# Kernel optimization log

Hardware: AMD Instinct MI355X
Metric: run time of the kernel (lower is better)

Reference implementation:

```python
import jax, jax.numpy as jnp
import numpy as np

FP8_MAX = 448.0  # e4m3 max, from scale = max(w) / (448.0 * 6.0) in the source


def setup_inputs() -> dict:
    key = jax.random.key(0)
    k_w, k_perm, k_x, k_b = jax.random.split(key, 4)
    T, K, O = 8192, 4096, 4096  # tokens = bsz*q_len, in_features, out_features

    # --- simulate init-time reorder_quantize_w ---
    w = jax.random.normal(k_w, (O, K), dtype=jnp.float32) * 0.02
    g_scale = jnp.max(jnp.abs(w)) / (FP8_MAX * 6.0)          # global weight scale
    perm = jax.random.permutation(k_perm, K)                  # outlier reorder index
    w_r = w[:, perm] / g_scale                                # reordered, globally scaled
    scale_w = jnp.max(jnp.abs(w_r), axis=1) / FP8_MAX         # per-out-channel scale (O,)
    W = jnp.round(w_r / scale_w[:, None])                     # quantized values (stored fp32)

    # --- simulate activation quantization (same reorder applied upstream) ---
    x = jax.random.normal(k_x, (T, K), dtype=jnp.float32)
    scale_x = (jnp.max(jnp.abs(x), axis=1, keepdims=True) / FP8_MAX)  # (T,1)
    qx = jnp.round(x / scale_x)                               # quantized values (stored fp32)

    bias = jax.random.normal(k_b, (O,), dtype=jnp.float32) * 0.01
    scale = jnp.asarray([g_scale], dtype=jnp.float32)         # fused global scale (x-global * w-global)

    return {"qx": qx, "W": W, "scale_x": scale_x, "scale_w": scale_w,
            "scale": scale, "bias": bias, "bsz": 4, "q_len": 2048}


def reference(qx, W, scale_x, scale_w, scale, bias, bsz, q_len):
    # agemm.matmul: low-bit GEMM with fused per-token (scale_x), per-channel (scale_w)
    # and global (scale) dequant scales.  y[t,o] = (sum_k qx[t,k]*W[o,k]) * sx[t] * sw[o] * s
    y = jnp.einsum('tk,ok->to', qx, W)           # (T, O) accumulate
    y = y * scale_x * scale_w[None, :] * scale[0]
    y = y + bias
    return y.reshape(bsz, q_len, -1)
```

## Files before the change

kernel.cpp:

```cpp
#include <hip/hip_runtime.h>

typedef __bf16 bf16_t;
typedef __bf16 bf16x8 __attribute__((ext_vector_type(8)));
typedef __bf16 bf16x4 __attribute__((ext_vector_type(4)));
typedef float f32x4 __attribute__((ext_vector_type(4)));

constexpr int TDIM = 8192;
constexpr int KDIM = 4096;
constexpr int ODIM = 4096;
constexpr int BM = 128, BN = 128, BK = 32;

__device__ __forceinline__ void async_ld16(void* lds, const void* g) {
    __builtin_amdgcn_global_load_lds(
        (const __attribute__((address_space(1))) unsigned int*)g,
        (__attribute__((address_space(3))) unsigned int*)lds,
        16, 0, 0);
}

__global__ __launch_bounds__(256) void cvt2_kernel(const float* __restrict__ a, bf16_t* __restrict__ da,
                                                   int nblk_a,
                                                   const float* __restrict__ w, bf16_t* __restrict__ dw) {
    int b = blockIdx.x;
    const float* src;
    bf16_t* dst;
    if (b < nblk_a) { src = a; dst = da; }
    else            { src = w; dst = dw; b -= nblk_a; }
    const size_t base = (size_t)b * 2048 + threadIdx.x * 4;
    const float4 v0 = *(const float4*)(src + base);
    const float4 v1 = *(const float4*)(src + base + 1024);
    bf16x4 o0, o1;
    o0[0] = (bf16_t)v0.x; o0[1] = (bf16_t)v0.y; o0[2] = (bf16_t)v0.z; o0[3] = (bf16_t)v0.w;
    o1[0] = (bf16_t)v1.x; o1[1] = (bf16_t)v1.y; o1[2] = (bf16_t)v1.z; o1[3] = (bf16_t)v1.w;
    *(bf16x4*)(dst + base) = o0;
    *(bf16x4*)(dst + base + 1024) = o1;
}

template <bool USE_DMA>
__global__ __launch_bounds__(256, 4) void gemm_kernel(
    const bf16_t* __restrict__ A, const bf16_t* __restrict__ B,
    const float* __restrict__ Afp, const float* __restrict__ Bfp,
    const float* __restrict__ scale_x, const float* __restrict__ scale_w,
    const float* __restrict__ gscale, const float* __restrict__ bias,
    float* __restrict__ out) {
    __shared__ bf16_t sA[BM * BK];
    __shared__ bf16_t sB[BN * BK];

    const int tid = threadIdx.x;
    const int bn = blockIdx.x & 31;
    const int bm = blockIdx.x >> 5;
    const int row0 = bm * BM;
    const int col0 = bn * BN;

    const int lane = tid & 63;
    const int wid = tid >> 6;
    const int wm = (wid >> 1) * 64;
    const int wn = (wid & 1) * 64;
    const int fr = lane & 15;
    const int q  = lane >> 4;
    const int s_fr = (fr >> 1) & 3;
    const int kc = ((q ^ s_fr) * 8);

    f32x4 acc[4][4] = {};

    const int r_half = tid >> 2;
    const int c_g = (tid & 3) ^ ((tid >> 3) & 3);
    const size_t a_g = (size_t)(row0 + r_half) * KDIM + c_g * 8;
    const size_t b_g = (size_t)(col0 + r_half) * KDIM + c_g * 8;
    const int lds_off = tid * 8;

    for (int k0 = 0; k0 < KDIM; k0 += BK) {
        if (USE_DMA) {
            async_ld16(&sA[lds_off],        A + a_g + k0);
            async_ld16(&sA[2048 + lds_off], A + a_g + (size_t)64 * KDIM + k0);
            async_ld16(&sB[lds_off],        B + b_g + k0);
            async_ld16(&sB[2048 + lds_off], B + b_g + (size_t)64 * KDIM + k0);
        } else {
            const int r = tid >> 2;
            const int cg2 = (tid & 3) ^ ((tid >> 3) & 3);
#pragma unroll
            for (int h = 0; h < 2; ++h) {
                const int rr = r + h * 64;
                const float4 va0 = *(const float4*)(Afp + (size_t)(row0 + rr) * KDIM + k0 + cg2 * 8);
                const float4 va1 = *(const float4*)(Afp + (size_t)(row0 + rr) * KDIM + k0 + cg2 * 8 + 4);
                const float4 vb0 = *(const float4*)(Bfp + (size_t)(col0 + rr) * KDIM + k0 + cg2 * 8);
                const float4 vb1 = *(const float4*)(Bfp + (size_t)(col0 + rr) * KDIM + k0 + cg2 * 8 + 4);
                bf16x8 pa, pb;
                pa[0] = (bf16_t)va0.x; pa[1] = (bf16_t)va0.y; pa[2] = (bf16_t)va0.z; pa[3] = (bf16_t)va0.w;
                pa[4] = (bf16_t)va1.x; pa[5] = (bf16_t)va1.y; pa[6] = (bf16_t)va1.z; pa[7] = (bf16_t)va1.w;
                pb[0] = (bf16_t)vb0.x; pb[1] = (bf16_t)vb0.y; pb[2] = (bf16_t)vb0.z; pb[3] = (bf16_t)vb0.w;
                pb[4] = (bf16_t)vb1.x; pb[5] = (bf16_t)vb1.y; pb[6] = (bf16_t)vb1.z; pb[7] = (bf16_t)vb1.w;
                *(bf16x8*)&sA[rr * BK + (tid & 3) * 8] = pa;
                *(bf16x8*)&sB[rr * BK + (tid & 3) * 8] = pb;
            }
        }
        __syncthreads();

        bf16x8 af[4], bfr[4];
#pragma unroll
        for (int mt = 0; mt < 4; ++mt)
            af[mt] = *(const bf16x8*)&sA[(wm + mt * 16 + fr) * BK + kc];
#pragma unroll
        for (int nt = 0; nt < 4; ++nt)
            bfr[nt] = *(const bf16x8*)&sB[(wn + nt * 16 + fr) * BK + kc];
#pragma unroll
        for (int mt = 0; mt < 4; ++mt)
#pragma unroll
            for (int nt = 0; nt < 4; ++nt)
                acc[mt][nt] = __builtin_amdgcn_mfma_f32_16x16x32_bf16(af[mt], bfr[nt], acc[mt][nt], 0, 0, 0);
        __syncthreads();
    }

    const float gs = gscale[0];
    const int rbase = q * 4;
#pragma unroll
    for (int nt = 0; nt < 4; ++nt) {
        const int o = col0 + wn + nt * 16 + fr;
        const float swv = scale_w[o] * gs;
        const float bv = bias[o];
#pragma unroll
        for (int mt = 0; mt < 4; ++mt) {
#pragma unroll
            for (int i = 0; i < 4; ++i) {
                const int t = row0 + wm + mt * 16 + rbase + i;
                out[(size_t)t * ODIM + o] = acc[mt][nt][i] * (scale_x[t] * swv) + bv;
            }
        }
    }
}

extern "C" void kernel_launch(void* const* d_in, const int* in_sizes, int n_in,
                              void* d_out, int out_size, void* d_ws, size_t ws_size,
                              hipStream_t stream) {
    const float* qx   = (const float*)d_in[0];
    const float* W    = (const float*)d_in[1];
    const float* sx   = (const float*)d_in[2];
    const float* sw   = (const float*)d_in[3];
    const float* gs   = (const float*)d_in[4];
    const float* bias = (const float*)d_in[5];
    float* out = (float*)d_out;

    const size_t nA = (size_t)TDIM * KDIM;
    const size_t nW = (size_t)ODIM * KDIM;
    const dim3 grid(2048);

    if (ws_size >= (nA + nW) * sizeof(bf16_t)) {
        bf16_t* Abf = (bf16_t*)d_ws;
        bf16_t* Wbf = Abf + nA;
        const int nblk_a = (int)(nA / 2048);
        const int nblk_w = (int)(nW / 2048);
        cvt2_kernel<<<dim3(nblk_a + nblk_w), dim3(256), 0, stream>>>(qx, Abf, nblk_a, W, Wbf);
        gemm_kernel<true><<<grid, dim3(256), 0, stream>>>(
            Abf, Wbf, nullptr, nullptr, sx, sw, gs, bias, out);
    } else {
        gemm_kernel<false><<<grid, dim3(256), 0, stream>>>(
            nullptr, nullptr, qx, W, sx, sw, gs, bias, out);
    }
}
```

Before: 568.4 us.

## Replace bf16 GEMM with 256x256 8-wave double-buffered pipelined kernel

The main GEMM moves from 128x128x32 tiles with 4 waves to 256x256x64 tiles with 8 waves. A two-stage LDS double buffer (128 KB) issues async global-to-LDS loads interleaved with MFMA phases, gated by explicit barriers, waitcnts, sched_barriers and setprio. Block indices are remapped for L2 locality and an XOR swizzle is used for LDS. The larger tiles raise arithmetic intensity and the interleaved prefetch is meant to hide load latency, at the cost of much higher register and LDS pressure and fragile hand scheduling.

```diff
diff --git a/kernel.cpp b/kernel.cpp
--- a/kernel.cpp
+++ b/kernel.cpp
@@ -8,7 +8,6 @@
 constexpr int TDIM = 8192;
 constexpr int KDIM = 4096;
 constexpr int ODIM = 4096;
-constexpr int BM = 128, BN = 128, BK = 32;
 
 __device__ __forceinline__ void async_ld16(void* lds, const void* g) {
     __builtin_amdgcn_global_load_lds(
@@ -35,21 +34,154 @@
     *(bf16x4*)(dst + base + 1024) = o1;
 }
 
-template <bool USE_DMA>
-__global__ __launch_bounds__(256, 4) void gemm_kernel(
+constexpr int BM = 256, BN = 256, BK = 64;
+constexpr int NKT = KDIM / BK;
+constexpr int NIT = NKT / 2;
+
+#define BAR   __builtin_amdgcn_s_barrier()
+#define SCB   __builtin_amdgcn_sched_barrier(0)
+#define WLG   asm volatile("s_waitcnt lgkmcnt(0)" ::: "memory")
+#define WV6   asm volatile("s_waitcnt vmcnt(6)" ::: "memory")
+#define WV0   asm volatile("s_waitcnt vmcnt(0)" ::: "memory")
+#define PRIO1 __builtin_amdgcn_s_setprio(1)
+#define PRIO0 __builtin_amdgcn_s_setprio(0)
+
+#define STG_A(c, kt, h) \
+    async_ld16(lds_a + (c)*32768 + (h)*16384,        a_srcb + (size_t)((h)*128     )*KDIM + (kt)*64); \
+    async_ld16(lds_a + (c)*32768 + (h)*16384 + 8192, a_srcb + (size_t)((h)*128 + 64)*KDIM + (kt)*64)
+#define STG_B(c, kt, h) \
+    async_ld16(lds_b + (c)*32768 + (h)*16384,        b_srcb + (size_t)((h)*128     )*KDIM + (kt)*64); \
+    async_ld16(lds_b + (c)*32768 + (h)*16384 + 8192, b_srcb + (size_t)((h)*128 + 64)*KDIM + (kt)*64)
+
+#define LD_A_LO(c) _Pragma("unroll") for (int m = 0; m < 4; ++m) { \
+    af[m][0] = *(const bf16x8*)(a_rd + (c)*32768 + m*2048 + ck0); \
+    af[m][1] = *(const bf16x8*)(a_rd + (c)*32768 + m*2048 + ck1); }
+#define LD_A_HI(c) _Pragma("unroll") for (int m = 0; m < 4; ++m) { \
+    af[m][0] = *(const bf16x8*)(a_rd + (c)*32768 + (m+4)*2048 + ck0); \
+    af[m][1] = *(const bf16x8*)(a_rd + (c)*32768 + (m+4)*2048 + ck1); }
+#define LD_B_ALL(c) _Pragma("unroll") for (int n = 0; n < 4; ++n) { \
+    bfr[n][0] = *(const bf16x8*)(b_rd + (c)*32768 + n*2048 + ck0); \
+    bfr[n][1] = *(const bf16x8*)(b_rd + (c)*32768 + n*2048 + ck1); }
+
+#define MFMA16(MB, NB) \
+  _Pragma("unroll") for (int m = 0; m < 4; ++m) \
+  _Pragma("unroll") for (int n = 0; n < 2; ++n) \
+  _Pragma("unroll") for (int k = 0; k < 2; ++k) \
+    acc[(MB)+m][(NB)+n] = __builtin_amdgcn_mfma_f32_16x16x32_bf16( \
+        af[m][k], bfr[(NB)+n][k], acc[(MB)+m][(NB)+n], 0, 0, 0)
+
+__global__ __launch_bounds__(512, 2) void gemm8_kernel(
     const bf16_t* __restrict__ A, const bf16_t* __restrict__ B,
+    const float* __restrict__ scale_x, const float* __restrict__ scale_w,
+    const float* __restrict__ gscale, const float* __restrict__ bias,
+    float* __restrict__ out)
+{
+    __shared__ __attribute__((aligned(16))) char smem[131072];
+
+    const int tid = threadIdx.x;
+    const int lin = (blockIdx.x & 7) * 64 + (blockIdx.x >> 3);
+    const int row0 = (lin >> 4) * BM;
+    const int col0 = (lin & 15) * BN;
+
+    const int ld_row = tid >> 3;
+    const int ld_ch  = (tid & 7) ^ (ld_row & 7);
+    const bf16_t* a_srcb = A + (size_t)(row0 + ld_row) * KDIM + ld_ch * 8;
+    const bf16_t* b_srcb = B + (size_t)(col0 + ld_row) * KDIM + ld_ch * 8;
+    char* lds_a = smem + tid * 16;
+    char* lds_b = smem + 65536 + tid * 16;
+
+    const int lane = tid & 63;
+    const int wid  = tid >> 6;
+    const int wm   = wid >> 2;
+    const int wn   = wid & 3;
+    const int fr   = lane & 15;
+    const int q    = lane >> 4;
+    const int swz  = lane & 7;
+    const int ck0  = ((q ^ swz)) * 16;
+    const int ck1  = (((4 | q) ^ swz)) * 16;
+    const char* a_rd = smem + (wm * 128 + fr) * 128;
+    const char* b_rd = smem + 65536 + (wn * 64 + fr) * 128;
+
+    f32x4 acc[8][4] = {};
+    bf16x8 af[4][2], bfr[4][2];
+
+    STG_B(0, 0, 0); STG_B(0, 0, 1);
+    STG_A(0, 0, 0); STG_A(0, 0, 1);
+    STG_B(1, 1, 0); STG_B(1, 1, 1);
+    STG_A(1, 1, 0);
+    WV6; SCB; BAR; SCB;
+
+#pragma unroll 1
+    for (int i = 0; i < NIT; ++i) {
+        const int tp = 2 * i + 2;
+        const bool pf = (tp < NKT);
+        LD_A_LO(0); LD_B_ALL(0);
+        STG_A(1, 2 * i + 1, 1);
+        BAR; WLG; SCB;
+        PRIO1; MFMA16(0, 0); PRIO0; SCB; BAR; SCB;
+        if (pf) { STG_B(0, tp, 0); }
+        BAR; SCB;
+        PRIO1; MFMA16(0, 2); PRIO0; SCB; BAR; SCB;
+        LD_A_HI(0);
+        if (pf) { STG_B(0, tp, 1); }
+        BAR; WLG; SCB;
+        PRIO1; MFMA16(4, 0); PRIO0; SCB; BAR; SCB;
+        if (pf) { STG_A(0, tp, 0); }
+        BAR; SCB;
+        PRIO1; MFMA16(4, 2); PRIO0; SCB;
+        if (i + 1 < NIT) { WV6; } else { WV0; }
+        SCB; BAR; SCB;
+        LD_A_LO(1); LD_B_ALL(1);
+        if (pf) { STG_A(0, tp, 1); }
+        BAR; WLG; SCB;
+        PRIO1; MFMA16(0, 0); PRIO0; SCB; BAR; SCB;
+        if (pf) { STG_B(1, tp + 1, 0); }
+        BAR; SCB;
+        PRIO1; MFMA16(0, 2); PRIO0; SCB; BAR; SCB;
+        LD_A_HI(1);
+        if (pf) { STG_B(1, tp + 1, 1); }
+        BAR; WLG; SCB;
+        PRIO1; MFMA16(4, 0); PRIO0; SCB; BAR; SCB;
+        if (pf) { STG_A(1, tp + 1, 0); }
+        BAR; SCB;
+        PRIO1; MFMA16(4, 2); PRIO0; SCB;
+        WV6; SCB; BAR; SCB;
+    }
+
+    const float gs = gscale[0];
+    const int trow = row0 + wm * 128 + q * 4;
+    const int ocol = col0 + wn * 64 + fr;
+#pragma unroll
+    for (int nt = 0; nt < 4; ++nt) {
+        const int o = ocol + nt * 16;
+        const float sws = scale_w[o] * gs;
+        const float bv = bias[o];
+#pragma unroll
+        for (int mt = 0; mt < 8; ++mt) {
+#pragma unroll
+            for (int ii = 0; ii < 4; ++ii) {
+                const int t = trow + mt * 16 + ii;
+                out[(size_t)t * ODIM + o] = acc[mt][nt][ii] * (scale_x[t] * sws) + bv;
+            }
+        }
+    }
+}
+
+constexpr int FBM = 128, FBN = 128, FBK = 32;
+
+__global__ __launch_bounds__(256, 4) void gemm_fallback(
     const float* __restrict__ Afp, const float* __restrict__ Bfp,
     const float* __restrict__ scale_x, const float* __restrict__ scale_w,
     const float* __restrict__ gscale, const float* __restrict__ bias,
     float* __restrict__ out) {
-    __shared__ bf16_t sA[BM * BK];
-    __shared__ bf16_t sB[BN * BK];
+    __shared__ bf16_t sA[FBM * FBK];
+    __shared__ bf16_t sB[FBN * FBK];
 
     const int tid = threadIdx.x;
     const int bn = blockIdx.x & 31;
     const int bm = blockIdx.x >> 5;
-    const int row0 = bm * BM;
-    const int col0 = bn * BN;
+    const int row0 = bm * FBM;
+    const int col0 = bn * FBN;
 
     const int lane = tid & 63;
     const int wid = tid >> 6;
@@ -62,51 +194,38 @@
 
     f32x4 acc[4][4] = {};
 
-    const int r_half = tid >> 2;
-    const int c_g = (tid & 3) ^ ((tid >> 3) & 3);
-    const size_t a_g = (size_t)(row0 + r_half) * KDIM + c_g * 8;
-    const size_t b_g = (size_t)(col0 + r_half) * KDIM + c_g * 8;
-    const int lds_off = tid * 8;
-
-    for (int k0 = 0; k0 < KDIM; k0 += BK) {
-        if (USE_DMA) {
-            async_ld16(&sA[lds_off],        A + a_g + k0);
-            async_ld16(&sA[2048 + lds_off], A + a_g + (size_t)64 * KDIM + k0);
-            async_ld16(&sB[lds_off],        B + b_g + k0);
-            async_ld16(&sB[2048 + lds_off], B + b_g + (size_t)64 * KDIM + k0);
-        } else {
-            const int r = tid >> 2;
-            const int cg2 = (tid & 3) ^ ((tid >> 3) & 3);
-#pragma unroll
-            for (int h = 0; h < 2; ++h) {
-                const int rr = r + h * 64;
-                const float4 va0 = *(const float4*)(Afp + (size_t)(row0 + rr) * KDIM + k0 + cg2 * 8);
-                const float4 va1 = *(const float4*)(Afp + (size_t)(row0 + rr) * KDIM + k0 + cg2 * 8 + 4);
-                const float4 vb0 = *(const float4*)(Bfp + (size_t)(col0 + rr) * KDIM + k0 + cg2 * 8);
-                const float4 vb1 = *(const float4*)(Bfp + (size_t)(col0 + rr) * KDIM + k0 + cg2 * 8 + 4);
-                bf16x8 pa, pb;
-                pa[0] = (bf16_t)va0.x; pa[1] = (bf16_t)va0.y; pa[2] = (bf16_t)va0.z; pa[3] = (bf16_t)va0.w;
-                pa[4] = (bf16_t)va1.x; pa[5] = (bf16_t)va1.y; pa[6] = (bf16_t)va1.z; pa[7] = (bf16_t)va1.w;
-                pb[0] = (bf16_t)vb0.x; pb[1] = (bf16_t)vb0.y; pb[2] = (bf16_t)vb0.z; pb[3] = (bf16_t)vb0.w;
-                pb[4] = (bf16_t)vb1.x; pb[5] = (bf16_t)vb1.y; pb[6] = (bf16_t)vb1.z; pb[7] = (bf16_t)vb1.w;
-                *(bf16x8*)&sA[rr * BK + (tid & 3) * 8] = pa;
-                *(bf16x8*)&sB[rr * BK + (tid & 3) * 8] = pb;
-            }
+    for (int k0 = 0; k0 < KDIM; k0 += FBK) {
+        const int r = tid >> 2;
+        const int cg2 = (tid & 3) ^ ((tid >> 3) & 3);
+#pragma unroll
+        for (int h = 0; h < 2; ++h) {
+            const int rr = r + h * 64;
+            const float4 va0 = *(const float4*)(Afp + (size_t)(row0 + rr) * KDIM + k0 + cg2 * 8);
+            const float4 va1 = *(const float4*)(Afp + (size_t)(row0 + rr) * KDIM + k0 + cg2 * 8 + 4);
+            const float4 vb0 = *(const float4*)(Bfp + (size_t)(col0 + rr) * KDIM + k0 + cg2 * 8);
+            const float4 vb1 = *(const float4*)(Bfp + (size_t)(col0 + rr) * KDIM + k0 + cg2 * 8 + 4);
+            bf16x8 pa, pb;
+            pa[0] = (bf16_t)va0.x; pa[1] = (bf16_t)va0.y; pa[2] = (bf16_t)va0.z; pa[3] = (bf16_t)va0.w;
+            pa[4] = (bf16_t)va1.x; pa[5] = (bf16_t)va1.y; pa[6] = (bf16_t)va1.z; pa[7] = (bf16_t)va1.w;
+            pb[0] = (bf16_t)vb0.x; pb[1] = (bf16_t)vb0.y; pb[2] = (bf16_t)vb0.z; pb[3] = (bf16_t)vb0.w;
+            pb[4] = (bf16_t)vb1.x; pb[5] = (bf16_t)vb1.y; pb[6] = (bf16_t)vb1.z; pb[7] = (bf16_t)vb1.w;
+            *(bf16x8*)&sA[rr * FBK + (tid & 3) * 8] = pa;
+            *(bf16x8*)&sB[rr * FBK + (tid & 3) * 8] = pb;
         }
         __syncthreads();
 
-        bf16x8 af[4], bfr[4];
+        bf16x8 a8[4], b8[4];
 #pragma unroll
         for (int mt = 0; mt < 4; ++mt)
-            af[mt] = *(const bf16x8*)&sA[(wm + mt * 16 + fr) * BK + kc];
+            a8[mt] = *(const bf16x8*)&sA[(wm + mt * 16 + fr) * FBK + kc];
 #pragma unroll
         for (int nt = 0; nt < 4; ++nt)
-            bfr[nt] = *(const bf16x8*)&sB[(wn + nt * 16 + fr) * BK + kc];
+            b8[nt] = *(const bf16x8*)&sB[(wn + nt * 16 + fr) * FBK + kc];
 #pragma unroll
         for (int mt = 0; mt < 4; ++mt)
 #pragma unroll
             for (int nt = 0; nt < 4; ++nt)
-                acc[mt][nt] = __builtin_amdgcn_mfma_f32_16x16x32_bf16(af[mt], bfr[nt], acc[mt][nt], 0, 0, 0);
+                acc[mt][nt] = __builtin_amdgcn_mfma_f32_16x16x32_bf16(a8[mt], b8[nt], acc[mt][nt], 0, 0, 0);
         __syncthreads();
     }
 
@@ -141,7 +260,6 @@
 
     const size_t nA = (size_t)TDIM * KDIM;
     const size_t nW = (size_t)ODIM * KDIM;
-    const dim3 grid(2048);
 
     if (ws_size >= (nA + nW) * sizeof(bf16_t)) {
         bf16_t* Abf = (bf16_t*)d_ws;
@@ -149,10 +267,10 @@
         const int nblk_a = (int)(nA / 2048);
         const int nblk_w = (int)(nW / 2048);
         cvt2_kernel<<<dim3(nblk_a + nblk_w), dim3(256), 0, stream>>>(qx, Abf, nblk_a, W, Wbf);
-        gemm_kernel<true><<<grid, dim3(256), 0, stream>>>(
-            Abf, Wbf, nullptr, nullptr, sx, sw, gs, bias, out);
+        gemm8_kernel<<<dim3((TDIM / BM) * (ODIM / BN)), dim3(512), 0, stream>>>(
+            Abf, Wbf, sx, sw, gs, bias, out);
     } else {
-        gemm_kernel<false><<<grid, dim3(256), 0, stream>>>(
-            nullptr, nullptr, qx, W, sx, sw, gs, bias, out);
-    }
-}
+        gemm_fallback<<<dim3((TDIM / FBM) * (ODIM / FBN)), dim3(256), 0, stream>>>(
+            qx, W, sx, sw, gs, bias, out);
+    }
+}
```

Measured after the change: 493.9 us. 13.1% less time.
